# Optimization experiments

Hardware: AMD Instinct MI355X
Metric: run time of the kernel (lower is better)

The kernel has to match this reference:

```python
import jax, jax.numpy as jnp
import numpy as np

N_NODES = 10000
N_EDGES = 640000
IN_CH = 128
OUT_CH = 128


def setup_inputs() -> dict:
    key = jax.random.key(0)
    k1, k2, k3, k4 = jax.random.split(key, 4)
    x = jax.random.normal(k1, (N_NODES, IN_CH), dtype=jnp.float32)
    edge_index = jax.random.randint(k2, (2, N_EDGES), 0, N_NODES, dtype=jnp.int64)
    # nn.Linear(2*in_channels, out_channels): weight [out, 2*in], bias [out]
    bound = 1.0 / np.sqrt(2 * IN_CH)
    W = jax.random.uniform(k3, (OUT_CH, 2 * IN_CH), dtype=jnp.float32, minval=-bound, maxval=bound)
    b = jax.random.uniform(k4, (OUT_CH,), dtype=jnp.float32, minval=-bound, maxval=bound)
    return {"x": x, "W": W, "b": b, "edge_index": edge_index}


def reference(x, W, b, edge_index):
    # PyG convention: edge_index[0] = source j, edge_index[1] = target i
    src, dst = edge_index[0], edge_index[1]
    x_i = x[dst]                      # [E, C] target features
    x_j = x[src]                      # [E, C] source features
    feat = jnp.concatenate([x_i, x_j - x_i], axis=-1)  # [E, 2C]
    msg = feat @ W.T + b              # [E, out]
    out = jax.ops.segment_max(msg, dst, num_segments=x.shape[0])  # [N, out]
    # isolated nodes: PyG scatter-max yields 0, segment_max yields -inf
    return jnp.where(jnp.isfinite(out), out, 0.0)
```

## Files before the change

kernel.cpp:

```cpp
#include <hip/hip_runtime.h>
#include <math.h>

#define N_CH 128
#define NB_MAX 1024
#define ECHUNK 2048
#define GCHUNK 2048

__global__ __launch_bounds__(256) void prep_kernel(const float* __restrict__ W,
                                                   float* __restrict__ V1,
                                                   float* __restrict__ V2,
                                                   int* __restrict__ binCount,
                                                   int* __restrict__ binCursor,
                                                   int nb) {
    int i = blockIdx.x * 256 + threadIdx.x;
    if (i < N_CH * N_CH) {
        int k = i >> 7, o = i & 127;
        float w1 = W[o * 256 + k];
        float w2 = W[o * 256 + 128 + k];
        int ip = (k >> 2) * 512 + o * 4 + (k & 3);
        V1[ip] = w1 - w2;
        V2[ip] = w2;
    }
    if (i < nb) { binCount[i] = 0; binCursor[i] = 0; }
}

__global__ __launch_bounds__(256) void gemm_kernel(const float* __restrict__ x,
                                                   const float* __restrict__ V1,
                                                   const float* __restrict__ V2,
                                                   const float* __restrict__ bias,
                                                   const int* __restrict__ dst,
                                                   float* __restrict__ A,
                                                   unsigned short* __restrict__ Bh,
                                                   int* __restrict__ binCount,
                                                   int n_nodes, int n_edges, int nb) {
    __shared__ float xs[32][N_CH];
    __shared__ int h[NB_MAX];
    const int tid = threadIdx.x;
    const int bid = blockIdx.x;

    const int ebase = bid * ECHUNK;
    const int ecnt = min(ECHUNK, n_edges - ebase);
    for (int i = tid; i < nb; i += 256) h[i] = 0;
    __syncthreads();
    if (ecnt > 0) {
        const int j = tid * 8;
        if (j + 8 <= ecnt) {
            int4 d0 = *(const int4*)(dst + ebase + j);
            int4 d1 = *(const int4*)(dst + ebase + j + 4);
            atomicAdd(&h[d0.x >> 4], 1); atomicAdd(&h[d0.y >> 4], 1);
            atomicAdd(&h[d0.z >> 4], 1); atomicAdd(&h[d0.w >> 4], 1);
            atomicAdd(&h[d1.x >> 4], 1); atomicAdd(&h[d1.y >> 4], 1);
            atomicAdd(&h[d1.z >> 4], 1); atomicAdd(&h[d1.w >> 4], 1);
        } else {
            for (int q = j; q < min(j + 8, ecnt); ++q)
                atomicAdd(&h[dst[ebase + q] >> 4], 1);
        }
    }
    __syncthreads();
    for (int i = tid; i < nb; i += 256)
        if (h[i]) atomicAdd(&binCount[i], h[i]);

    const int n0 = bid * 32;
    if (n0 >= n_nodes) return;

    if (n0 + 32 <= n_nodes) {
        const float4* xg = (const float4*)(x + (size_t)n0 * N_CH);
        float4* xsv = (float4*)&xs[0][0];
        #pragma unroll
        for (int i = 0; i < 4; ++i) xsv[tid + i * 256] = xg[tid + i * 256];
    } else {
        for (int i = tid; i < 32 * N_CH; i += 256) {
            int n = n0 + (i >> 7);
            (&xs[0][0])[i] = (n < n_nodes) ? x[(size_t)n * N_CH + (i & 127)] : 0.f;
        }
    }
    __syncthreads();

    const int o  = tid & 127;
    const int nh = tid >> 7;
    const float bo = bias[o];
    float acc1[16], acc2[16];
    #pragma unroll
    for (int i = 0; i < 16; ++i) { acc1[i] = 0.f; acc2[i] = 0.f; }

    const float* xrow = &xs[nh * 16][0];
    for (int k4 = 0; k4 < N_CH; k4 += 4) {
        float4 w1 = *(const float4*)(V1 + k4 * 128 + o * 4);
        float4 w2 = *(const float4*)(V2 + k4 * 128 + o * 4);
        #pragma unroll
        for (int i = 0; i < 16; ++i) {
            float4 xv = *(const float4*)&xrow[i * N_CH + k4];
            acc1[i] = fmaf(xv.x, w1.x, acc1[i]); acc2[i] = fmaf(xv.x, w2.x, acc2[i]);
            acc1[i] = fmaf(xv.y, w1.y, acc1[i]); acc2[i] = fmaf(xv.y, w2.y, acc2[i]);
            acc1[i] = fmaf(xv.z, w1.z, acc1[i]); acc2[i] = fmaf(xv.z, w2.z, acc2[i]);
            acc1[i] = fmaf(xv.w, w1.w, acc1[i]); acc2[i] = fmaf(xv.w, w2.w, acc2[i]);
        }
    }

    #pragma unroll
    for (int i = 0; i < 16; ++i) {
        int n = n0 + nh * 16 + i;
        if (n < n_nodes) {
            A[(size_t)n * N_CH + o] = acc1[i] + bo;
            unsigned int bits = __float_as_uint(acc2[i]);
            unsigned int r = (bits + 0x7FFFu + ((bits >> 16) & 1u)) >> 16;
            Bh[(size_t)n * N_CH + o] = (unsigned short)r;
        }
    }
}

__global__ __launch_bounds__(256) void bin_kernel(const int* __restrict__ src,
                                                  const int* __restrict__ dst,
                                                  const int* __restrict__ binCount,
                                                  int* __restrict__ binCursor,
                                                  int* __restrict__ binOffG,
                                                  unsigned int* __restrict__ binned,
                                                  int n_edges, int nb) {
    __shared__ int sc[256];
    __shared__ int hist[NB_MAX];
    __shared__ int bOff[NB_MAX];
    const int tid = threadIdx.x;
    const int base = blockIdx.x * ECHUNK;
    const int cnt = min(ECHUNK, n_edges - base);

    int p[4]; int s = 0;
    #pragma unroll
    for (int k = 0; k < 4; ++k) {
        int slot = tid * 4 + k;
        int c = (slot < nb) ? binCount[slot] : 0;
        p[k] = (c + 3) & ~3;
        s += p[k];
    }
    sc[tid] = s;
    __syncthreads();
    #pragma unroll
    for (int off = 1; off < 256; off <<= 1) {
        int u = (tid >= off) ? sc[tid - off] : 0;
        __syncthreads();
        sc[tid] += u;
        __syncthreads();
    }
    int run = sc[tid] - s;
    #pragma unroll
    for (int k = 0; k < 4; ++k) {
        int slot = tid * 4 + k;
        bOff[slot] = run;
        run += p[k];
    }
    if (blockIdx.x == 0) {
        #pragma unroll
        for (int k = 0; k < 4; ++k) {
            int slot = tid * 4 + k;
            if (slot < nb) binOffG[slot] = bOff[slot];
        }
    }
    for (int i = tid; i < NB_MAX; i += 256) hist[i] = 0;
    __syncthreads();

    const int myb = tid * 8;
    const int mycnt = max(0, min(8, cnt - myb));
    unsigned int pk[8]; int bb[8], rr[8];
    if (mycnt == 8) {
        int4 s0 = *(const int4*)(src + base + myb);
        int4 s1 = *(const int4*)(src + base + myb + 4);
        int4 d0 = *(const int4*)(dst + base + myb);
        int4 d1 = *(const int4*)(dst + base + myb + 4);
        int sv[8] = {s0.x, s0.y, s0.z, s0.w, s1.x, s1.y, s1.z, s1.w};
        int dv[8] = {d0.x, d0.y, d0.z, d0.w, d1.x, d1.y, d1.z, d1.w};
        #pragma unroll
        for (int k = 0; k < 8; ++k) {
            int b = dv[k] >> 4;
            pk[k] = ((unsigned int)(dv[k] & 15) << 14) | (unsigned int)sv[k];
            bb[k] = b;
            rr[k] = atomicAdd(&hist[b], 1);
        }
    } else {
        for (int k = 0; k < mycnt; ++k) {
            int sv = src[base + myb + k];
            int dv = dst[base + myb + k];
            int b = dv >> 4;
            pk[k] = ((unsigned int)(dv & 15) << 14) | (unsigned int)sv;
            bb[k] = b;
            rr[k] = atomicAdd(&hist[b], 1);
        }
    }
    __syncthreads();

    for (int i = tid; i < nb; i += 256) {
        int c = hist[i];
        if (c) bOff[i] += atomicAdd(&binCursor[i], c);
    }
    __syncthreads();

    for (int k = 0; k < mycnt; ++k)
        binned[bOff[bb[k]] + rr[k]] = pk[k];
}

#define FOLD4(acc_lo, acc_hi, a, b, c, d)                                        \
    acc_lo = fmaxf(acc_lo, fmaxf(fmaxf(__uint_as_float((a) << 16),               \
                                       __uint_as_float((b) << 16)),              \
                                 fmaxf(__uint_as_float((c) << 16),               \
                                       __uint_as_float((d) << 16))));            \
    acc_hi = fmaxf(acc_hi, fmaxf(fmaxf(__uint_as_float((a) & 0xFFFF0000u),       \
                                       __uint_as_float((b) & 0xFFFF0000u)),      \
                                 fmaxf(__uint_as_float((c) & 0xFFFF0000u),       \
                                       __uint_as_float((d) & 0xFFFF0000u))));

__global__ __launch_bounds__(256) void gather_kernel(
        const float* __restrict__ A,
        const uint4* __restrict__ Bh4,
        const int* __restrict__ binOffG,
        const int* __restrict__ binCount,
        const unsigned int* __restrict__ binned,
        float* __restrict__ out,
        int n_nodes) {
    __shared__ int lidx[GCHUNK];
    __shared__ int h16[16], e17[17];
    const int b = blockIdx.x;
    const int tid = threadIdx.x;
    const int wv  = tid >> 6;
    const int l   = tid & 63;
    const int sub = l >> 4;
    const int col = l & 15;
    const int rbeg = binOffG[b];
    const int cnt  = binCount[b];

    float mlo[4][4], mhi[4][4]; int tcnt[4];
    #pragma unroll
    for (int i = 0; i < 4; ++i) {
        tcnt[i] = 0;
        #pragma unroll
        for (int u = 0; u < 4; ++u) { mlo[i][u] = -INFINITY; mhi[i][u] = -INFINITY; }
    }

    for (int cb = 0; cb < cnt; cb += GCHUNK) {
        const int ccnt = min(GCHUNK, cnt - cb);
        if (tid < 16) h16[tid] = 0;
        __syncthreads();

        const int mb = tid * 8;
        const int mc = max(0, min(8, ccnt - mb));
        int myd[8], mys[8], myr[8];
        if (mc == 8) {
            int4 r0 = *(const int4*)((const int*)binned + rbeg + cb + mb);
            int4 r1 = *(const int4*)((const int*)binned + rbeg + cb + mb + 4);
            unsigned int wv8[8] = {(unsigned int)r0.x, (unsigned int)r0.y,
                                   (unsigned int)r0.z, (unsigned int)r0.w,
                                   (unsigned int)r1.x, (unsigned int)r1.y,
                                   (unsigned int)r1.z, (unsigned int)r1.w};
            #pragma unroll
            for (int k = 0; k < 8; ++k) {
                myd[k] = (int)(wv8[k] >> 14);
                mys[k] = (int)(wv8[k] & 16383u);
                myr[k] = atomicAdd(&h16[myd[k]], 1);
            }
        } else {
            for (int k = 0; k < mc; ++k) {
                unsigned int w = binned[rbeg + cb + mb + k];
                myd[k] = (int)(w >> 14);
                mys[k] = (int)(w & 16383u);
                myr[k] = atomicAdd(&h16[myd[k]], 1);
            }
        }
        __syncthreads();
        if (tid == 0) {
            int s = 0;
            #pragma unroll
            for (int k = 0; k < 16; ++k) { e17[k] = s; s += h16[k]; }
            e17[16] = s;
        }
        __syncthreads();
        for (int k = 0; k < mc; ++k)
            lidx[e17[myd[k]] + myr[k]] = mys[k];
        __syncthreads();

        #pragma unroll
        for (int i = 0; i < 4; ++i) {
            const int nl = wv * 4 + i;
            const int c  = h16[nl];
            const int bg = e17[nl];
            tcnt[i] += c;
            int q = 0;
            for (; q + 16 <= c; q += 16) {
                int e0 = lidx[bg + q + sub];
                int e1 = lidx[bg + q + 4 + sub];
                int e2 = lidx[bg + q + 8 + sub];
                int e3 = lidx[bg + q + 12 + sub];
                uint4 w0 = Bh4[(size_t)e0 * 16 + col];
                uint4 w1 = Bh4[(size_t)e1 * 16 + col];
                uint4 w2 = Bh4[(size_t)e2 * 16 + col];
                uint4 w3 = Bh4[(size_t)e3 * 16 + col];
                FOLD4(mlo[i][0], mhi[i][0], w0.x, w1.x, w2.x, w3.x);
                FOLD4(mlo[i][1], mhi[i][1], w0.y, w1.y, w2.y, w3.y);
                FOLD4(mlo[i][2], mhi[i][2], w0.z, w1.z, w2.z, w3.z);
                FOLD4(mlo[i][3], mhi[i][3], w0.w, w1.w, w2.w, w3.w);
            }
            for (; q < c; q += 4) {
                int r = q + sub;
                if (r < c) {
                    uint4 w = Bh4[(size_t)lidx[bg + r] * 16 + col];
                    mlo[i][0] = fmaxf(mlo[i][0], __uint_as_float(w.x << 16));
                    mhi[i][0] = fmaxf(mhi[i][0], __uint_as_float(w.x & 0xFFFF0000u));
                    mlo[i][1] = fmaxf(mlo[i][1], __uint_as_float(w.y << 16));
                    mhi[i][1] = fmaxf(mhi[i][1], __uint_as_float(w.y & 0xFFFF0000u));
                    mlo[i][2] = fmaxf(mlo[i][2], __uint_as_float(w.z << 16));
                    mhi[i][2] = fmaxf(mhi[i][2], __uint_as_float(w.z & 0xFFFF0000u));
                    mlo[i][3] = fmaxf(mlo[i][3], __uint_as_float(w.w << 16));
                    mhi[i][3] = fmaxf(mhi[i][3], __uint_as_float(w.w & 0xFFFF0000u));
                }
            }
        }
        __syncthreads();
    }

    #pragma unroll
    for (int i = 0; i < 4; ++i) {
        const int n = b * 16 + wv * 4 + i;
        if (n >= n_nodes) continue;
        float lo[4], hi[4];
        #pragma unroll
        for (int u = 0; u < 4; ++u) {
            lo[u] = mlo[i][u]; hi[u] = mhi[i][u];
            lo[u] = fmaxf(lo[u], __shfl_xor(lo[u], 16, 64));
            hi[u] = fmaxf(hi[u], __shfl_xor(hi[u], 16, 64));
            lo[u] = fmaxf(lo[u], __shfl_xor(lo[u], 32, 64));
            hi[u] = fmaxf(hi[u], __shfl_xor(hi[u], 32, 64));
        }
        if (sub == 0) {
            float r8[8];
            if (tcnt[i] > 0) {
                const float4* Arow = (const float4*)(A + (size_t)n * N_CH + col * 8);
                float4 a0 = Arow[0], a1 = Arow[1];
                r8[0] = a0.x + lo[0]; r8[1] = a0.y + hi[0];
                r8[2] = a0.z + lo[1]; r8[3] = a0.w + hi[1];
                r8[4] = a1.x + lo[2]; r8[5] = a1.y + hi[2];
                r8[6] = a1.z + lo[3]; r8[7] = a1.w + hi[3];
            } else {
                #pragma unroll
                for (int j = 0; j < 8; ++j) r8[j] = 0.f;
            }
            float4* orow = (float4*)(out + (size_t)n * N_CH + col * 8);
            orow[0] = make_float4(r8[0], r8[1], r8[2], r8[3]);
            orow[1] = make_float4(r8[4], r8[5], r8[6], r8[7]);
        }
    }
}

extern "C" void kernel_launch(void* const* d_in, const int* in_sizes, int n_in,
                              void* d_out, int out_size, void* d_ws, size_t ws_size,
                              hipStream_t stream) {
    const float* x = (const float*)d_in[0];
    const float* W = (const float*)d_in[1];
    const float* b = (const float*)d_in[2];
    const int*   ei = (const int*)d_in[3];

    const int n_nodes = in_sizes[0] / N_CH;
    const int n_edges = in_sizes[3] / 2;
    const int nb = (n_nodes + 15) >> 4;
    const int* src = ei;
    const int* dst = ei + n_edges;
    float* out = (float*)d_out;

    char* ws = (char*)d_ws;
    size_t off = 0;
    auto alloc = [&](size_t bytes) -> void* {
        void* p = ws + off;
        off += (bytes + 255) & ~(size_t)255;
        return p;
    };
    float* V1        = (float*)alloc((size_t)N_CH * N_CH * 4);
    float* V2        = (float*)alloc((size_t)N_CH * N_CH * 4);
    float* A         = (float*)alloc((size_t)n_nodes * N_CH * 4);
    unsigned short* Bh = (unsigned short*)alloc((size_t)n_nodes * N_CH * 2);
    int*   binCount  = (int*)alloc((size_t)nb * 4);
    int*   binCursor = (int*)alloc((size_t)nb * 4);
    int*   binOffG   = (int*)alloc((size_t)nb * 4);
    unsigned int* binned = (unsigned int*)alloc(((size_t)n_edges + 4 * NB_MAX) * 4);
    (void)ws_size; (void)n_in; (void)out_size;

    const int nodeBlocks = (n_nodes + 31) / 32;
    const int edgeBlocks = (n_edges + ECHUNK - 1) / ECHUNK;
    const int ng = max(nodeBlocks, edgeBlocks);

    prep_kernel  <<<64, 256, 0, stream>>>(W, V1, V2, binCount, binCursor, nb);
    gemm_kernel  <<<ng, 256, 0, stream>>>(x, V1, V2, b, dst, A, Bh, binCount,
                                          n_nodes, n_edges, nb);
    bin_kernel   <<<edgeBlocks, 256, 0, stream>>>(src, dst, binCount, binCursor,
                                                  binOffG, binned, n_edges, nb);
    gather_kernel<<<nb, 256, 0, stream>>>(A, (const uint4*)Bh, binOffG, binCount,
                                          binned, out, n_nodes);
}
```

Baseline: 133.8 us.

## Move bin prefix scan into last gemm block and halve chunk sizes

The exclusive scan over per-bin counts, which every bin_kernel block used to recompute redundantly, now runs once in the last-finishing gemm block, detected with a global done counter and threadfence. That block writes the bin offsets and cursors. ECHUNK and the per-block node tile are halved, giving more, smaller blocks for both the gemm and the binning kernels. This removes the repeated scan and shared-memory pressure in bin_kernel, but adds a serial tail in gemm_kernel and more global atomics on bin counts.

```diff
diff --git a/kernel.cpp b/kernel.cpp
--- a/kernel.cpp
+++ b/kernel.cpp
@@ -3,14 +3,14 @@
 
 #define N_CH 128
 #define NB_MAX 1024
-#define ECHUNK 2048
+#define ECHUNK 1024
 #define GCHUNK 2048
 
 __global__ __launch_bounds__(256) void prep_kernel(const float* __restrict__ W,
                                                    float* __restrict__ V1,
                                                    float* __restrict__ V2,
                                                    int* __restrict__ binCount,
-                                                   int* __restrict__ binCursor,
+                                                   int* __restrict__ done,
                                                    int nb) {
     int i = blockIdx.x * 256 + threadIdx.x;
     if (i < N_CH * N_CH) {
@@ -21,7 +21,8 @@
         V1[ip] = w1 - w2;
         V2[ip] = w2;
     }
-    if (i < nb) { binCount[i] = 0; binCursor[i] = 0; }
+    if (i < nb) binCount[i] = 0;
+    if (i == 0) *done = 0;
 }
 
 __global__ __launch_bounds__(256) void gemm_kernel(const float* __restrict__ x,
@@ -32,9 +33,14 @@
                                                    float* __restrict__ A,
                                                    unsigned short* __restrict__ Bh,
                                                    int* __restrict__ binCount,
+                                                   int* __restrict__ binOffG,
+                                                   int* __restrict__ binCursor,
+                                                   int* __restrict__ done,
                                                    int n_nodes, int n_edges, int nb) {
-    __shared__ float xs[32][N_CH];
+    __shared__ float xs[16][N_CH];
     __shared__ int h[NB_MAX];
+    __shared__ int sc[256];
+    __shared__ int isLast;
     const int tid = threadIdx.x;
     const int bid = blockIdx.x;
 
@@ -43,16 +49,13 @@
     for (int i = tid; i < nb; i += 256) h[i] = 0;
     __syncthreads();
     if (ecnt > 0) {
-        const int j = tid * 8;
-        if (j + 8 <= ecnt) {
-            int4 d0 = *(const int4*)(dst + ebase + j);
-            int4 d1 = *(const int4*)(dst + ebase + j + 4);
-            atomicAdd(&h[d0.x >> 4], 1); atomicAdd(&h[d0.y >> 4], 1);
-            atomicAdd(&h[d0.z >> 4], 1); atomicAdd(&h[d0.w >> 4], 1);
-            atomicAdd(&h[d1.x >> 4], 1); atomicAdd(&h[d1.y >> 4], 1);
-            atomicAdd(&h[d1.z >> 4], 1); atomicAdd(&h[d1.w >> 4], 1);
+        const int j = tid * 4;
+        if (j + 4 <= ecnt) {
+            int4 d4 = *(const int4*)(dst + ebase + j);
+            atomicAdd(&h[d4.x >> 4], 1); atomicAdd(&h[d4.y >> 4], 1);
+            atomicAdd(&h[d4.z >> 4], 1); atomicAdd(&h[d4.w >> 4], 1);
         } else {
-            for (int q = j; q < min(j + 8, ecnt); ++q)
+            for (int q = j; q < ecnt; ++q)
                 atomicAdd(&h[dst[ebase + q] >> 4], 1);
         }
     }
@@ -60,124 +63,118 @@
     for (int i = tid; i < nb; i += 256)
         if (h[i]) atomicAdd(&binCount[i], h[i]);
 
-    const int n0 = bid * 32;
-    if (n0 >= n_nodes) return;
-
-    if (n0 + 32 <= n_nodes) {
-        const float4* xg = (const float4*)(x + (size_t)n0 * N_CH);
-        float4* xsv = (float4*)&xs[0][0];
-        #pragma unroll
-        for (int i = 0; i < 4; ++i) xsv[tid + i * 256] = xg[tid + i * 256];
-    } else {
-        for (int i = tid; i < 32 * N_CH; i += 256) {
-            int n = n0 + (i >> 7);
-            (&xs[0][0])[i] = (n < n_nodes) ? x[(size_t)n * N_CH + (i & 127)] : 0.f;
-        }
-    }
-    __syncthreads();
-
-    const int o  = tid & 127;
-    const int nh = tid >> 7;
-    const float bo = bias[o];
-    float acc1[16], acc2[16];
+    const int n0 = bid * 16;
+    if (n0 < n_nodes) {
+        if (n0 + 16 <= n_nodes) {
+            const float4* xg = (const float4*)(x + (size_t)n0 * N_CH);
+            float4* xsv = (float4*)&xs[0][0];
+            xsv[tid] = xg[tid];
+            xsv[tid + 256] = xg[tid + 256];
+        } else {
+            for (int i = tid; i < 16 * N_CH; i += 256) {
+                int n = n0 + (i >> 7);
+                (&xs[0][0])[i] = (n < n_nodes) ? x[(size_t)n * N_CH + (i & 127)] : 0.f;
+            }
+        }
+        __syncthreads();
+
+        const int o  = tid & 127;
+        const int nh = tid >> 7;
+        const float bo = bias[o];
+        float acc1[8], acc2[8];
+        #pragma unroll
+        for (int i = 0; i < 8; ++i) { acc1[i] = 0.f; acc2[i] = 0.f; }
+
+        const float* xrow = &xs[nh * 8][0];
+        for (int k4 = 0; k4 < N_CH; k4 += 4) {
+            float4 w1 = *(const float4*)(V1 + k4 * 128 + o * 4);
+            float4 w2 = *(const float4*)(V2 + k4 * 128 + o * 4);
+            #pragma unroll
+            for (int i = 0; i < 8; ++i) {
+                float4 xv = *(const float4*)&xrow[i * N_CH + k4];
+                acc1[i] = fmaf(xv.x, w1.x, acc1[i]); acc2[i] = fmaf(xv.x, w2.x, acc2[i]);
+                acc1[i] = fmaf(xv.y, w1.y, acc1[i]); acc2[i] = fmaf(xv.y, w2.y, acc2[i]);
+                acc1[i] = fmaf(xv.z, w1.z, acc1[i]); acc2[i] = fmaf(xv.z, w2.z, acc2[i]);
+                acc1[i] = fmaf(xv.w, w1.w, acc1[i]); acc2[i] = fmaf(xv.w, w2.w, acc2[i]);
+            }
+        }
+
+        #pragma unroll
+        for (int i = 0; i < 8; ++i) {
+            int n = n0 + nh * 8 + i;
+            if (n < n_nodes) {
+                A[(size_t)n * N_CH + o] = acc1[i] + bo;
+                unsigned int bits = __float_as_uint(acc2[i]);
+                unsigned int r = (bits + 0x7FFFu + ((bits >> 16) & 1u)) >> 16;
+                Bh[(size_t)n * N_CH + o] = (unsigned short)r;
+            }
+        }
+    }
+
+    __threadfence();
+    __syncthreads();
+    if (tid == 0) isLast = (atomicAdd(done, 1) == (int)gridDim.x - 1) ? 1 : 0;
+    __syncthreads();
+    if (!isLast) return;
+
+    const int npt = (nb + 255) >> 8;
+    int pv[4]; int s = 0;
+    for (int k = 0; k < npt; ++k) {
+        int slot = tid * npt + k;
+        int c = (slot < nb) ? atomicAdd(&binCount[slot], 0) : 0;
+        pv[k] = (c + 3) & ~3;
+        s += pv[k];
+    }
+    sc[tid] = s;
+    __syncthreads();
     #pragma unroll
-    for (int i = 0; i < 16; ++i) { acc1[i] = 0.f; acc2[i] = 0.f; }
-
-    const float* xrow = &xs[nh * 16][0];
-    for (int k4 = 0; k4 < N_CH; k4 += 4) {
-        float4 w1 = *(const float4*)(V1 + k4 * 128 + o * 4);
-        float4 w2 = *(const float4*)(V2 + k4 * 128 + o * 4);
-        #pragma unroll
-        for (int i = 0; i < 16; ++i) {
-            float4 xv = *(const float4*)&xrow[i * N_CH + k4];
-            acc1[i] = fmaf(xv.x, w1.x, acc1[i]); acc2[i] = fmaf(xv.x, w2.x, acc2[i]);
-            acc1[i] = fmaf(xv.y, w1.y, acc1[i]); acc2[i] = fmaf(xv.y, w2.y, acc2[i]);
-            acc1[i] = fmaf(xv.z, w1.z, acc1[i]); acc2[i] = fmaf(xv.z, w2.z, acc2[i]);
-            acc1[i] = fmaf(xv.w, w1.w, acc1[i]); acc2[i] = fmaf(xv.w, w2.w, acc2[i]);
-        }
-    }
-
-    #pragma unroll
-    for (int i = 0; i < 16; ++i) {
-        int n = n0 + nh * 16 + i;
-        if (n < n_nodes) {
-            A[(size_t)n * N_CH + o] = acc1[i] + bo;
-            unsigned int bits = __float_as_uint(acc2[i]);
-            unsigned int r = (bits + 0x7FFFu + ((bits >> 16) & 1u)) >> 16;
-            Bh[(size_t)n * N_CH + o] = (unsigned short)r;
-        }
+    for (int off = 1; off < 256; off <<= 1) {
+        int u = (tid >= off) ? sc[tid - off] : 0;
+        __syncthreads();
+        sc[tid] += u;
+        __syncthreads();
+    }
+    int run = sc[tid] - s;
+    for (int k = 0; k < npt; ++k) {
+        int slot = tid * npt + k;
+        if (slot < nb) { binOffG[slot] = run; binCursor[slot] = run; }
+        run += pv[k];
     }
 }
 
 __global__ __launch_bounds__(256) void bin_kernel(const int* __restrict__ src,
                                                   const int* __restrict__ dst,
-                                                  const int* __restrict__ binCount,
                                                   int* __restrict__ binCursor,
-                                                  int* __restrict__ binOffG,
                                                   unsigned int* __restrict__ binned,
                                                   int n_edges, int nb) {
-    __shared__ int sc[256];
     __shared__ int hist[NB_MAX];
-    __shared__ int bOff[NB_MAX];
+    __shared__ int rbase[NB_MAX];
     const int tid = threadIdx.x;
     const int base = blockIdx.x * ECHUNK;
     const int cnt = min(ECHUNK, n_edges - base);
 
-    int p[4]; int s = 0;
-    #pragma unroll
-    for (int k = 0; k < 4; ++k) {
-        int slot = tid * 4 + k;
-        int c = (slot < nb) ? binCount[slot] : 0;
-        p[k] = (c + 3) & ~3;
-        s += p[k];
-    }
-    sc[tid] = s;
-    __syncthreads();
-    #pragma unroll
-    for (int off = 1; off < 256; off <<= 1) {
-        int u = (tid >= off) ? sc[tid - off] : 0;
-        __syncthreads();
-        sc[tid] += u;
-        __syncthreads();
-    }
-    int run = sc[tid] - s;
-    #pragma unroll
-    for (int k = 0; k < 4; ++k) {
-        int slot = tid * 4 + k;
-        bOff[slot] = run;
-        run += p[k];
-    }
-    if (blockIdx.x == 0) {
+    for (int i = tid; i < nb; i += 256) hist[i] = 0;
+    __syncthreads();
+
+    const int j = tid * 4;
+    const int mc = max(0, min(4, cnt - j));
+    unsigned int pk[4]; int bb[4], rr[4];
+    if (mc == 4) {
+        int4 s4 = *(const int4*)(src + base + j);
+        int4 d4 = *(const int4*)(dst + base + j);
+        int sv[4] = {s4.x, s4.y, s4.z, s4.w};
+        int dv[4] = {d4.x, d4.y, d4.z, d4.w};
         #pragma unroll
         for (int k = 0; k < 4; ++k) {
-            int slot = tid * 4 + k;
-            if (slot < nb) binOffG[slot] = bOff[slot];
-        }
-    }
-    for (int i = tid; i < NB_MAX; i += 256) hist[i] = 0;
-    __syncthreads();
-
-    const int myb = tid * 8;
-    const int mycnt = max(0, min(8, cnt - myb));
-    unsigned int pk[8]; int bb[8], rr[8];
-    if (mycnt == 8) {
-        int4 s0 = *(const int4*)(src + base + myb);
-        int4 s1 = *(const int4*)(src + base + myb + 4);
-        int4 d0 = *(const int4*)(dst + base + myb);
-        int4 d1 = *(const int4*)(dst + base + myb + 4);
-        int sv[8] = {s0.x, s0.y, s0.z, s0.w, s1.x, s1.y, s1.z, s1.w};
-        int dv[8] = {d0.x, d0.y, d0.z, d0.w, d1.x, d1.y, d1.z, d1.w};
-        #pragma unroll
-        for (int k = 0; k < 8; ++k) {
             int b = dv[k] >> 4;
             pk[k] = ((unsigned int)(dv[k] & 15) << 14) | (unsigned int)sv[k];
             bb[k] = b;
             rr[k] = atomicAdd(&hist[b], 1);
         }
     } else {
-        for (int k = 0; k < mycnt; ++k) {
-            int sv = src[base + myb + k];
-            int dv = dst[base + myb + k];
+        for (int k = 0; k < mc; ++k) {
+            int sv = src[base + j + k];
+            int dv = dst[base + j + k];
             int b = dv >> 4;
             pk[k] = ((unsigned int)(dv & 15) << 14) | (unsigned int)sv;
             bb[k] = b;
@@ -188,12 +185,12 @@
 
     for (int i = tid; i < nb; i += 256) {
         int c = hist[i];
-        if (c) bOff[i] += atomicAdd(&binCursor[i], c);
-    }
-    __syncthreads();
-
-    for (int k = 0; k < mycnt; ++k)
-        binned[bOff[bb[k]] + rr[k]] = pk[k];
+        if (c) rbase[i] = atomicAdd(&binCursor[i], c);
+    }
+    __syncthreads();
+
+    for (int k = 0; k < mc; ++k)
+        binned[rbase[bb[k]] + rr[k]] = pk[k];
 }
 
 #define FOLD4(acc_lo, acc_hi, a, b, c, d)                                        \
@@ -337,7 +334,7 @@
                 r8[6] = a1.z + lo[3]; r8[7] = a1.w + hi[3];
             } else {
                 #pragma unroll
-                for (int j = 0; j < 8; ++j) r8[j] = 0.f;
+                for (int j2 = 0; j2 < 8; ++j2) r8[j2] = 0.f;
             }
             float4* orow = (float4*)(out + (size_t)n * N_CH + col * 8);
             orow[0] = make_float4(r8[0], r8[1], r8[2], r8[3]);
@@ -375,18 +372,20 @@
     int*   binCount  = (int*)alloc((size_t)nb * 4);
     int*   binCursor = (int*)alloc((size_t)nb * 4);
     int*   binOffG   = (int*)alloc((size_t)nb * 4);
+    int*   done      = (int*)alloc(256);
     unsigned int* binned = (unsigned int*)alloc(((size_t)n_edges + 4 * NB_MAX) * 4);
     (void)ws_size; (void)n_in; (void)out_size;
 
-    const int nodeBlocks = (n_nodes + 31) / 32;
-    const int edgeBlocks = (n_edges + ECHUNK - 1) / ECHUNK;
-    const int ng = max(nodeBlocks, edgeBlocks);
-
-    prep_kernel  <<<64, 256, 0, stream>>>(W, V1, V2, binCount, binCursor, nb);
+    const int nodeChunks = (n_nodes + 15) >> 4;
+    const int edgeChunks = (n_edges + ECHUNK - 1) / ECHUNK;
+    const int ng = max(nodeChunks, edgeChunks);
+
+    prep_kernel  <<<64, 256, 0, stream>>>(W, V1, V2, binCount, done, nb);
     gemm_kernel  <<<ng, 256, 0, stream>>>(x, V1, V2, b, dst, A, Bh, binCount,
+                                          binOffG, binCursor, done,
                                           n_nodes, n_edges, nb);
-    bin_kernel   <<<edgeBlocks, 256, 0, stream>>>(src, dst, binCount, binCursor,
-                                                  binOffG, binned, n_edges, nb);
+    bin_kernel   <<<edgeChunks, 256, 0, stream>>>(src, dst, binCursor, binned,
+                                                  n_edges, nb);
     gather_kernel<<<nb, 256, 0, stream>>>(A, (const uint4*)Bh, binOffG, binCount,
                                           binned, out, n_nodes);
 }
```

Result: slower. 200.6 us (+49.9%).
